# Optimization experiments

Measured on AMD Instinct MI355X. Metric: run time of the kernel, lower is better.

## Reference

```python
import jax, jax.numpy as jnp
import numpy as np

N, FEATS, CLASSES, E = 100000, 32, 16, 1600000
EMB_DIM = 1 + int(np.log2(FEATS))  # 6
HIDDEN = 3 + EMB_DIM               # 9
DEPTH = 10
DIFF = 0.9


def setup_inputs() -> dict:
    key = jax.random.key(0)
    ks = jax.random.split(key, 10)
    s = lambda k, *sh: jax.random.normal(k, sh, dtype=jnp.float32)
    return {
        "x": s(ks[0], N, FEATS),
        "edges": jax.random.randint(ks[1], (2, E), 0, N, dtype=jnp.int64),
        "emb_table": s(ks[2], FEATS, EMB_DIM) * 0.1,
        "W1": s(ks[3], 1 + EMB_DIM, HIDDEN) * 0.3,
        "b1": jnp.zeros((HIDDEN,), jnp.float32),
        "W2": s(ks[4], HIDDEN, 1) * 0.3,
        "b2": jnp.zeros((1,), jnp.float32),
        "Wout": s(ks[5], FEATS, CLASSES) * 0.1,
        "bout": jnp.zeros((CLASSES,), jnp.float32),
    }


def reference(x, edges, emb_table, W1, b1, W2, b2, Wout, bout):
    n, f = x.shape
    src, dst = edges[0], edges[1]
    # symmetric degree normalization (parameter-free GraphConv)
    deg = jax.ops.segment_sum(jnp.ones((src.shape[0],), x.dtype), dst, num_segments=n)
    deg = jnp.maximum(deg, 1.0)
    norm = jax.lax.rsqrt(deg[src] * deg[dst])  # [E]

    def conv(h):
        return jax.ops.segment_sum(h[src] * norm[:, None], dst, num_segments=n)

    def diffuse(h):
        h0 = h
        for _ in range(DEPTH):
            h = conv(h) * DIFF + (1.0 - DIFF) * h0
        return h

    x = diffuse(x)
    # per-(node, class) MLP: x.t().reshape(-1,1) orders rows class-major
    col = x.T.reshape(-1, 1)                       # [f*n, 1]
    emb = jnp.repeat(emb_table, n, axis=0)         # [f*n, EMB_DIM] (class cl repeated n times)
    h = jnp.concatenate([col, emb], axis=1)        # [f*n, 1+EMB_DIM]
    h = jax.nn.relu(h @ W1 + b1)
    h = h @ W2 + b2                                # [f*n, 1]
    x = h.reshape(f, n).T                          # [n, f]
    x = diffuse(x)
    return x @ Wout + bout
```

## Files before the change

kernel.cpp:

```cpp
#include <hip/hip_runtime.h>
#include <hip/hip_fp16.h>

#define ELL_CAP 64
#define NSLICE 8
#define EPB 2048


__global__ __launch_bounds__(256) void ell_fill(
    const int* __restrict__ edges, int* __restrict__ deg,
    int* __restrict__ ell, int e, int n, int slice_sz) {
    int slice = blockIdx.x & (NSLICE - 1);
    int chunk = blockIdx.x >> 3;
    int lo = slice * slice_sz;
    int hi = min(n, lo + slice_sz);
    int base = chunk * EPB + threadIdx.x;
    int d[EPB / 256], s[EPB / 256];
#pragma unroll
    for (int k = 0; k < EPB / 256; ++k) {
        int i = base + k * 256;
        int valid = i < e;
        int ii = valid ? i : 0;
        int dv = edges[e + ii];
        int sv = edges[ii];
        d[k] = valid ? dv : -1;
        s[k] = sv;
    }
#pragma unroll
    for (int k = 0; k < EPB / 256; ++k) {
        int dv = d[k];
        if (dv < lo || dv >= hi) continue;
        int slot = atomicAdd(&deg[dv], 1);
        if (slot < ELL_CAP) ell[((size_t)dv << 6) + slot] = s[k];
    }
}

__global__ void nodeconst_kernel(const int* __restrict__ deg, float* __restrict__ rs,
                                 float* __restrict__ sq, float* __restrict__ wdeg,
                                 int* __restrict__ ell, int n) {
    int i = blockIdx.x * blockDim.x + threadIdx.x;
    if (i > n) return;
    int v = (i < n) ? deg[i] : 0;
    float d = (float)max(v, 1);
    float r = rsqrtf(d);
    rs[i] = r;
    sq[i] = sqrtf(d);
    wdeg[i] = 0.9f * r * r;
    if (i < n) {
        int dg = min(v, ELL_CAP);
        int dgp = (dg + 7) & ~7;
        for (int k = dg; k < dgp; ++k) ell[((size_t)i << 6) + k] = n;
    }
}

__global__ void prescale_kernel(const float2* __restrict__ x2, const float* __restrict__ rs,
                                __half2* __restrict__ g, int n) {
    int i = blockIdx.x * blockDim.x + threadIdx.x;
    int node = i >> 4;
    if (node > n) return;
    if (node == n) { g[i] = __floats2half2_rn(0.f, 0.f); return; }
    float2 v = x2[i];
    float r = rs[node];
    g[i] = __floats2half2_rn(v.x * r, v.y * r);
}


union H4 {
    uint2 u;
    __half2 h[2];
};

__global__ __launch_bounds__(256) void conv_kernel(
    const uint2* __restrict__ gin, const uint2* __restrict__ g0,
    uint2* __restrict__ gout, const int* __restrict__ deg,
    const int* __restrict__ ell, const float* __restrict__ wdeg, int n) {
    int gid = blockIdx.x * blockDim.x + threadIdx.x;
    int node = gid >> 3;
    int q = gid & 7;
    if (node > n) return;
    int dg = (node < n) ? min(deg[node], ELL_CAP) : 0;
    int trips = (dg + 7) >> 3;
    int j0 = node << 6;
    float w = wdeg[node];
    H4 g0v;
    g0v.u = g0[gid];
    float ax = 0.f, ay = 0.f, az = 0.f, aw = 0.f;
    __half2 b0l = __floats2half2_rn(0.f, 0.f), b0h = b0l;
    __half2 b1l = b0l, b1h = b0l;
    __half2 b2l = b0l, b2h = b0l;
    __half2 b3l = b0l, b3h = b0l;
    int scur = ell[j0 + q];
    for (int r = 0; r < trips; ++r) {
        int snext = ell[j0 + (r + 1) * 8 + q];
        int s0 = __shfl(scur, 0, 8), s1 = __shfl(scur, 1, 8);
        int s2 = __shfl(scur, 2, 8), s3 = __shfl(scur, 3, 8);
        int s4 = __shfl(scur, 4, 8), s5 = __shfl(scur, 5, 8);
        int s6 = __shfl(scur, 6, 8), s7 = __shfl(scur, 7, 8);
        H4 v0, v1, v2, v3, v4, v5, v6, v7;
        v0.u = gin[(size_t)s0 * 8 + q];
        v1.u = gin[(size_t)s1 * 8 + q];
        v2.u = gin[(size_t)s2 * 8 + q];
        v3.u = gin[(size_t)s3 * 8 + q];
        v4.u = gin[(size_t)s4 * 8 + q];
        v5.u = gin[(size_t)s5 * 8 + q];
        v6.u = gin[(size_t)s6 * 8 + q];
        v7.u = gin[(size_t)s7 * 8 + q];
        b0l = __hadd2(b0l, v0.h[0]); b0h = __hadd2(b0h, v0.h[1]);
        b1l = __hadd2(b1l, v1.h[0]); b1h = __hadd2(b1h, v1.h[1]);
        b2l = __hadd2(b2l, v2.h[0]); b2h = __hadd2(b2h, v2.h[1]);
        b3l = __hadd2(b3l, v3.h[0]); b3h = __hadd2(b3h, v3.h[1]);
        b0l = __hadd2(b0l, v4.h[0]); b0h = __hadd2(b0h, v4.h[1]);
        b1l = __hadd2(b1l, v5.h[0]); b1h = __hadd2(b1h, v5.h[1]);
        b2l = __hadd2(b2l, v6.h[0]); b2h = __hadd2(b2h, v6.h[1]);
        b3l = __hadd2(b3l, v7.h[0]); b3h = __hadd2(b3h, v7.h[1]);
        if (r & 1) {
            float2 t;
            t = __half22float2(b0l); ax += t.x; ay += t.y;
            t = __half22float2(b0h); az += t.x; aw += t.y;
            t = __half22float2(b1l); ax += t.x; ay += t.y;
            t = __half22float2(b1h); az += t.x; aw += t.y;
            t = __half22float2(b2l); ax += t.x; ay += t.y;
            t = __half22float2(b2h); az += t.x; aw += t.y;
            t = __half22float2(b3l); ax += t.x; ay += t.y;
            t = __half22float2(b3h); az += t.x; aw += t.y;
            b0l = __floats2half2_rn(0.f, 0.f); b0h = b0l;
            b1l = b0l; b1h = b0l;
            b2l = b0l; b2h = b0l;
            b3l = b0l; b3h = b0l;
        }
        scur = snext;
    }
    {
        float2 t;
        t = __half22float2(b0l); ax += t.x; ay += t.y;
        t = __half22float2(b0h); az += t.x; aw += t.y;
        t = __half22float2(b1l); ax += t.x; ay += t.y;
        t = __half22float2(b1h); az += t.x; aw += t.y;
        t = __half22float2(b2l); ax += t.x; ay += t.y;
        t = __half22float2(b2h); az += t.x; aw += t.y;
        t = __half22float2(b3l); ax += t.x; ay += t.y;
        t = __half22float2(b3h); az += t.x; aw += t.y;
    }
    float2 g0lo = __half22float2(g0v.h[0]);
    float2 g0hi = __half22float2(g0v.h[1]);
    float rx = w * ax + 0.1f * g0lo.x;
    float ry = w * ay + 0.1f * g0lo.y;
    float rz = w * az + 0.1f * g0hi.x;
    float rw = w * aw + 0.1f * g0hi.y;
    H4 o;
    o.h[0] = __floats2half2_rn(rx, ry);
    o.h[1] = __floats2half2_rn(rz, rw);
    gout[gid] = o.u;
}


__global__ __launch_bounds__(256) void mlp_kernel(
    const __half* __restrict__ gin, __half* __restrict__ gout,
    const float* __restrict__ rs, const float* __restrict__ sq,
    const float* __restrict__ emb,
    const float* __restrict__ W1,
    const float* __restrict__ b1,
    const float* __restrict__ W2,
    const float* __restrict__ b2,
    int n) {
    __shared__ float c[32][9];
    __shared__ float w0[9], w2[9];
    __shared__ float b2s;
    int tid = threadIdx.x;
    for (int i = tid; i < 288; i += blockDim.x) {
        int f = i / 9, jj = i % 9;
        float acc = b1[jj];
#pragma unroll
        for (int k = 0; k < 6; ++k) acc += emb[f * 6 + k] * W1[(1 + k) * 9 + jj];
        c[f][jj] = acc;
    }
    if (tid < 9) { w0[tid] = W1[tid]; w2[tid] = W2[tid]; }
    if (tid == 0) b2s = b2[0];
    __syncthreads();
    int gid = blockIdx.x * blockDim.x + tid;
    int node = gid >> 5;
    if (node > n) return;
    if (node == n) { gout[gid] = __float2half_rn(0.f); return; }
    int f = gid & 31;
    float xv = __half2float(gin[gid]) * sq[node];
    float acc = b2s;
#pragma unroll
    for (int jj = 0; jj < 9; ++jj)
        acc += fmaxf(xv * w0[jj] + c[f][jj], 0.0f) * w2[jj];
    gout[gid] = __float2half_rn(acc * rs[node]);
}


__global__ __launch_bounds__(256) void out_kernel(
    const __half* __restrict__ g, const float* __restrict__ sq,
    const float* __restrict__ Wout, const float* __restrict__ bout,
    float* __restrict__ out, int n) {
    __shared__ float w[32 * 16];
    __shared__ float bo[16];
    int tid = threadIdx.x;
    for (int i = tid; i < 512; i += blockDim.x) w[i] = Wout[i];
    if (tid < 16) bo[tid] = bout[tid];
    __syncthreads();
    int gid = blockIdx.x * blockDim.x + tid;
    int node = gid >> 4;
    int cls = gid & 15;
    if (node >= n) return;
    const __half* gr = g + (size_t)node * 32;
    float acc = 0.0f;
#pragma unroll
    for (int f = 0; f < 32; ++f) acc += __half2float(gr[f]) * w[f * 16 + cls];
    out[gid] = acc * sq[node] + bo[cls];
}

extern "C" void kernel_launch(void* const* d_in, const int* in_sizes, int n_in,
                              void* d_out, int out_size, void* d_ws, size_t ws_size,
                              hipStream_t stream) {
    const float* x    = (const float*)d_in[0];
    const int* edges  = (const int*)d_in[1];
    const float* emb  = (const float*)d_in[2];
    const float* W1   = (const float*)d_in[3];
    const float* b1   = (const float*)d_in[4];
    const float* W2   = (const float*)d_in[5];
    const float* b2   = (const float*)d_in[6];
    const float* Wout = (const float*)d_in[7];
    const float* bout = (const float*)d_in[8];
    float* out        = (float*)d_out;

    const int N = in_sizes[0] / 32;
    const int E = in_sizes[1] / 2;

    size_t off = 0;
    auto walloc = [&](size_t bytes) {
        void* p = (char*)d_ws + off;
        off += (bytes + 255) & ~(size_t)255;
        return p;
    };
    int*     deg   = (int*)    walloc((size_t)(N + 1) * 4);
    float*   rs    = (float*)  walloc((size_t)(N + 1) * 4);
    float*   sq    = (float*)  walloc((size_t)(N + 1) * 4);
    float*   wdeg  = (float*)  walloc((size_t)(N + 1) * 4);
    int*     ell   = (int*)    walloc((size_t)(N + 1) * ELL_CAP * 4 + 256);
    __half*  g0buf = (__half*) walloc((size_t)(N + 1) * 32 * 2);
    __half*  bufA  = (__half*) walloc((size_t)(N + 1) * 32 * 2);
    __half*  bufB  = (__half*) walloc((size_t)(N + 1) * 32 * 2);

    hipMemsetAsync(deg, 0, (size_t)(N + 1) * 4, stream);
    {
        int slice_sz = (N + NSLICE - 1) / NSLICE;
        int chunks = (E + EPB - 1) / EPB;
        ell_fill<<<chunks * NSLICE, 256, 0, stream>>>(edges, deg, ell, E, N, slice_sz);
    }
    nodeconst_kernel<<<(N + 1 + 255) / 256, 256, 0, stream>>>(deg, rs, sq, wdeg, ell, N);

    const int conv_blocks = ((N + 1) * 8 + 255) / 256;
    const int elem_blocks = ((N + 1) * 32 + 255) / 256;
    const int pair_blocks = ((N + 1) * 16 + 255) / 256;

    prescale_kernel<<<pair_blocks, 256, 0, stream>>>((const float2*)x, rs,
                                                     (__half2*)g0buf, N);

    {
        const uint2* gin = (const uint2*)g0buf;
        for (int it = 0; it < 10; ++it) {
            uint2* go = (uint2*)((it & 1) ? bufB : bufA);
            conv_kernel<<<conv_blocks, 256, 0, stream>>>(gin, (const uint2*)g0buf, go,
                                                         deg, ell, wdeg, N);
            gin = go;
        }
    }
    mlp_kernel<<<elem_blocks, 256, 0, stream>>>(bufB, g0buf, rs, sq, emb, W1, b1, W2, b2, N);

    {
        const uint2* gin = (const uint2*)g0buf;
        for (int it = 0; it < 10; ++it) {
            uint2* go = (uint2*)((it & 1) ? bufB : bufA);
            conv_kernel<<<conv_blocks, 256, 0, stream>>>(gin, (const uint2*)g0buf, go,
                                                         deg, ell, wdeg, N);
            gin = go;
        }
    }
    out_kernel<<<(N * 16 + 255) / 256, 256, 0, stream>>>(bufB, sq, Wout, bout, out, N);
}
```

Before: 626.9 us.

## Replace fixed-stride ELL adjacency with slice-allocated padded CSR

```diff
diff --git a/kernel.cpp b/kernel.cpp
--- a/kernel.cpp
+++ b/kernel.cpp
@@ -1,18 +1,64 @@
 #include <hip/hip_runtime.h>
 #include <hip/hip_fp16.h>
 
-#define ELL_CAP 64
 #define NSLICE 8
 #define EPB 2048
 
 
-__global__ __launch_bounds__(256) void ell_fill(
+__global__ __launch_bounds__(256) void count_kernel(
     const int* __restrict__ edges, int* __restrict__ deg,
-    int* __restrict__ ell, int e, int n, int slice_sz) {
+    int e, int n, int slice_sz) {
     int slice = blockIdx.x & (NSLICE - 1);
     int chunk = blockIdx.x >> 3;
     int lo = slice * slice_sz;
     int hi = min(n, lo + slice_sz);
+    int base = chunk * EPB + threadIdx.x;
+    int d[EPB / 256];
+#pragma unroll
+    for (int k = 0; k < EPB / 256; ++k) {
+        int i = base + k * 256;
+        int valid = i < e;
+        int ii = valid ? i : 0;
+        int dv = edges[e + ii];
+        d[k] = valid ? dv : -1;
+    }
+#pragma unroll
+    for (int k = 0; k < EPB / 256; ++k) {
+        int dv = d[k];
+        if (dv < lo || dv >= hi) continue;
+        atomicAdd(&deg[dv], 1);
+    }
+}
+
+__global__ void nodeconst_kernel(const int* __restrict__ deg, int* __restrict__ alloc8,
+                                 float* __restrict__ rs, float* __restrict__ sq,
+                                 float* __restrict__ wdeg, int* __restrict__ rowp,
+                                 int* __restrict__ cur, int* __restrict__ col,
+                                 int n, int slice_sz, int rcap) {
+    int i = blockIdx.x * blockDim.x + threadIdx.x;
+    if (i > n) return;
+    int v = (i < n) ? deg[i] : 0;
+    float d = (float)max(v, 1);
+    float r = rsqrtf(d);
+    rs[i] = r;
+    sq[i] = sqrtf(d);
+    wdeg[i] = 0.9f * r * r;
+    int p = (v + 7) & ~7;
+    int slice = (i < n) ? (i / slice_sz) : 0;
+    int base = slice * rcap + atomicAdd(&alloc8[slice], p);
+    rowp[i] = base;
+    cur[i] = base;
+    for (int k = v; k < p; ++k) col[base + k] = n;
+}
+
+__global__ __launch_bounds__(256) void csr_fill(
+    const int* __restrict__ edges, int* __restrict__ cur,
+    int* __restrict__ col, int e, int n, int slice_sz, int rcap) {
+    int slice = blockIdx.x & (NSLICE - 1);
+    int chunk = blockIdx.x >> 3;
+    int lo = slice * slice_sz;
+    int hi = min(n, lo + slice_sz);
+    int lim = (slice + 1) * rcap;
     int base = chunk * EPB + threadIdx.x;
     int d[EPB / 256], s[EPB / 256];
 #pragma unroll
@@ -29,26 +75,8 @@
     for (int k = 0; k < EPB / 256; ++k) {
         int dv = d[k];
         if (dv < lo || dv >= hi) continue;
-        int slot = atomicAdd(&deg[dv], 1);
-        if (slot < ELL_CAP) ell[((size_t)dv << 6) + slot] = s[k];
-    }
-}
-
-__global__ void nodeconst_kernel(const int* __restrict__ deg, float* __restrict__ rs,
-                                 float* __restrict__ sq, float* __restrict__ wdeg,
-                                 int* __restrict__ ell, int n) {
-    int i = blockIdx.x * blockDim.x + threadIdx.x;
-    if (i > n) return;
-    int v = (i < n) ? deg[i] : 0;
-    float d = (float)max(v, 1);
-    float r = rsqrtf(d);
-    rs[i] = r;
-    sq[i] = sqrtf(d);
-    wdeg[i] = 0.9f * r * r;
-    if (i < n) {
-        int dg = min(v, ELL_CAP);
-        int dgp = (dg + 7) & ~7;
-        for (int k = dg; k < dgp; ++k) ell[((size_t)i << 6) + k] = n;
+        int slot = atomicAdd(&cur[dv], 1);
+        if (slot < lim) col[slot] = s[k];
     }
 }
 
@@ -72,14 +100,15 @@
 __global__ __launch_bounds__(256) void conv_kernel(
     const uint2* __restrict__ gin, const uint2* __restrict__ g0,
     uint2* __restrict__ gout, const int* __restrict__ deg,
-    const int* __restrict__ ell, const float* __restrict__ wdeg, int n) {
+    const int* __restrict__ rowp, const int* __restrict__ col,
+    const float* __restrict__ wdeg, int n) {
     int gid = blockIdx.x * blockDim.x + threadIdx.x;
     int node = gid >> 3;
     int q = gid & 7;
     if (node > n) return;
-    int dg = (node < n) ? min(deg[node], ELL_CAP) : 0;
+    int dg = deg[node];
     int trips = (dg + 7) >> 3;
-    int j0 = node << 6;
+    int j0 = rowp[node];
     float w = wdeg[node];
     H4 g0v;
     g0v.u = g0[gid];
@@ -88,9 +117,9 @@
     __half2 b1l = b0l, b1h = b0l;
     __half2 b2l = b0l, b2h = b0l;
     __half2 b3l = b0l, b3h = b0l;
-    int scur = ell[j0 + q];
+    int scur = col[j0 + q];
     for (int r = 0; r < trips; ++r) {
-        int snext = ell[j0 + (r + 1) * 8 + q];
+        int snext = col[j0 + (r + 1) * 8 + q];
         int s0 = __shfl(scur, 0, 8), s1 = __shfl(scur, 1, 8);
         int s2 = __shfl(scur, 2, 8), s3 = __shfl(scur, 3, 8);
         int s4 = __shfl(scur, 4, 8), s5 = __shfl(scur, 5, 8);
@@ -228,28 +257,34 @@
     const int N = in_sizes[0] / 32;
     const int E = in_sizes[1] / 2;
 
+    const int slice_sz = (N + NSLICE - 1) / NSLICE;
+    const int RCAP = E / NSLICE + 8 * slice_sz + 4096;
+
     size_t off = 0;
     auto walloc = [&](size_t bytes) {
         void* p = (char*)d_ws + off;
         off += (bytes + 255) & ~(size_t)255;
         return p;
     };
-    int*     deg   = (int*)    walloc((size_t)(N + 1) * 4);
+    int*     deg   = (int*)    walloc((size_t)(N + 1 + 8) * 4);
+    int*     alloc8= deg + (N + 1);
     float*   rs    = (float*)  walloc((size_t)(N + 1) * 4);
     float*   sq    = (float*)  walloc((size_t)(N + 1) * 4);
     float*   wdeg  = (float*)  walloc((size_t)(N + 1) * 4);
-    int*     ell   = (int*)    walloc((size_t)(N + 1) * ELL_CAP * 4 + 256);
+    int*     rowp  = (int*)    walloc((size_t)(N + 1) * 4);
+    int*     cur   = (int*)    walloc((size_t)(N + 1) * 4);
+    int*     col   = (int*)    walloc((size_t)NSLICE * RCAP * 4 + 256);
     __half*  g0buf = (__half*) walloc((size_t)(N + 1) * 32 * 2);
     __half*  bufA  = (__half*) walloc((size_t)(N + 1) * 32 * 2);
     __half*  bufB  = (__half*) walloc((size_t)(N + 1) * 32 * 2);
 
-    hipMemsetAsync(deg, 0, (size_t)(N + 1) * 4, stream);
-    {
-        int slice_sz = (N + NSLICE - 1) / NSLICE;
-        int chunks = (E + EPB - 1) / EPB;
-        ell_fill<<<chunks * NSLICE, 256, 0, stream>>>(edges, deg, ell, E, N, slice_sz);
-    }
-    nodeconst_kernel<<<(N + 1 + 255) / 256, 256, 0, stream>>>(deg, rs, sq, wdeg, ell, N);
+    hipMemsetAsync(deg, 0, (size_t)(N + 1 + 8) * 4, stream);
+
+    const int chunks = (E + EPB - 1) / EPB;
+    count_kernel<<<chunks * NSLICE, 256, 0, stream>>>(edges, deg, E, N, slice_sz);
+    nodeconst_kernel<<<(N + 1 + 255) / 256, 256, 0, stream>>>(
+        deg, alloc8, rs, sq, wdeg, rowp, cur, col, N, slice_sz, RCAP);
+    csr_fill<<<chunks * NSLICE, 256, 0, stream>>>(edges, cur, col, E, N, slice_sz, RCAP);
 
     const int conv_blocks = ((N + 1) * 8 + 255) / 256;
     const int elem_blocks = ((N + 1) * 32 + 255) / 256;
@@ -263,7 +298,7 @@
         for (int it = 0; it < 10; ++it) {
             uint2* go = (uint2*)((it & 1) ? bufB : bufA);
             conv_kernel<<<conv_blocks, 256, 0, stream>>>(gin, (const uint2*)g0buf, go,
-                                                         deg, ell, wdeg, N);
+                                                         deg, rowp, col, wdeg, N);
             gin = go;
         }
     }
@@ -274,7 +309,7 @@
         for (int it = 0; it < 10; ++it) {
             uint2* go = (uint2*)((it & 1) ? bufB : bufA);
             conv_kernel<<<conv_blocks, 256, 0, stream>>>(gin, (const uint2*)g0buf, go,
-                                                         deg, ell, wdeg, N);
+                                                         deg, rowp, col, wdeg, N);
             gin = go;
         }
     }
```

Measured after the change: 1.834 ms. 2.92x slower.
